# Kernel tuning notes

Hardware: AMD Instinct MI355X
Metric: run time of the kernel (lower is better)

Reference implementation:

```python
import jax, jax.numpy as jnp
import numpy as np

MAX_REL = 30
N_HEADS = 8


def conv1d(x, w, b=None, groups=1):
    # x: [B, L, Cin], w: [Cout, Cin/groups, K]  (torch Conv1d layout), 'same' padding
    pad = w.shape[-1] // 2
    y = jax.lax.conv_general_dilated(
        x, w, window_strides=(1,), padding=[(pad, pad)],
        dimension_numbers=("NLC", "OIL", "NLC"), feature_group_count=groups)
    return y if b is None else y + b


def setup_inputs() -> dict:
    key = jax.random.key(0)
    ks = jax.random.split(key, 16)
    B, L, S = 8, 1024, 512          # L = 2 * S (required by Gamma.repeat(1,2,1))
    sd, vd, dm = 512, 64, 512       # spatial_dim == d_model (residual add)
    D = 3 * vd                      # rel-pos / K,V channel dim

    def n(k, shape, s):
        return (jax.random.normal(k, shape, jnp.float32) * s).astype(jnp.float32)

    return {
        "x_spatial": jax.random.normal(ks[0], (B, L, sd), jnp.float32),
        "x_velocity": jax.random.normal(ks[1], (B, S, vd), jnp.float32),
        "w_gamma": n(ks[2], (dm, vd, 1), 0.05)[:, :, 0],      # conv_gamma 1x1, no bias -> [dm, vd]
        "w3": n(ks[3], (vd, vd, 3), 0.07), "b3": jnp.zeros((vd,), jnp.float32),
        "w5": n(ks[4], (vd, vd, 5), 0.05), "b5": jnp.zeros((vd,), jnp.float32),
        "w7": n(ks[5], (vd, vd, 7), 0.04), "b7": jnp.zeros((vd,), jnp.float32),
        "rel_table": n(ks[6], (2 * MAX_REL + 1, D), 0.05),    # embedding [61, 192]
        "dw_w": n(ks[7], (D, 1, 3), 0.3), "dw_b": jnp.zeros((D,), jnp.float32),
        "wq": n(ks[8], (dm, sd), 0.03),
        "wk": n(ks[9], (dm, D), 0.05),
        "wv": n(ks[10], (dm, D), 0.05),
        "fc_w": n(ks[11], (dm, dm), 0.03), "fc_b": jnp.zeros((dm,), jnp.float32),
        "ln_g": jnp.ones((dm,), jnp.float32), "ln_b": jnp.zeros((dm,), jnp.float32),
    }


def rel_pos_enc(ms, rel_table, dw_w, dw_b):
    # Math-equivalent reduction of the torch O(B*S^2*D) op:
    # output[b,j] = mean_i where(i==j, dwconv_row_i(fused)[j], fused[b,i,j])
    #            = ms[b,j] + mean_i rel[i,j] + (diag_conv[b,j] - fused[b,j,j]) / S
    B, S, D = ms.shape
    pos = jnp.arange(S)
    idx = jnp.clip(pos[None, :] - pos[:, None], -MAX_REL, MAX_REL) + MAX_REL  # [S,S]
    mean_rel = rel_table[idx].mean(axis=0)                                    # [S,D]
    # fused[b,i,j] = ms[b,j] + rel_table[idx[i,j]]; diagonal uses idx = MAX_REL,
    # its +/-1 neighbors along j use MAX_REL -/+ ... -> rel[i,i-1]=MAX_REL-1, rel[i,i+1]=MAX_REL+1
    center = ms + rel_table[MAX_REL]                                          # fused[b,i,i]
    left = jnp.pad(ms[:, :-1] + rel_table[MAX_REL - 1], ((0, 0), (1, 0), (0, 0)))   # conv zero-pads at i=0
    right = jnp.pad(ms[:, 1:] + rel_table[MAX_REL + 1], ((0, 0), (0, 1), (0, 0)))   # conv zero-pads at i=S-1
    diag_conv = dw_w[:, 0, 0] * left + dw_w[:, 0, 1] * center + dw_w[:, 0, 2] * right + dw_b
    return ms + mean_rel[None] + (diag_conv - center) / S


def reference(x_spatial, x_velocity, w_gamma, w3, b3, w5, b5, w7, b7,
              rel_table, dw_w, dw_b, wq, wk, wv, fc_w, fc_b, ln_g, ln_b):
    B, S, vd = x_velocity.shape
    _, L, _ = x_spatial.shape
    dm = wq.shape[0]
    dk = dm // N_HEADS

    gamma = jax.nn.sigmoid(jnp.einsum("bsc,dc->bsd", x_velocity, w_gamma))   # [B,S,dm]

    ms = jnp.concatenate([conv1d(x_velocity, w3, b3),
                          conv1d(x_velocity, w5, b5),
                          conv1d(x_velocity, w7, b7)], axis=-1)              # [B,S,3vd]
    x_pe = rel_pos_enc(ms, rel_table, dw_w, dw_b)                            # [B,S,3vd]

    q = jnp.einsum("blc,dc->bld", x_spatial, wq).reshape(B, L, N_HEADS, dk).transpose(0, 2, 1, 3)
    k = jnp.einsum("bsc,dc->bsd", x_pe, wk).reshape(B, S, N_HEADS, dk).transpose(0, 2, 1, 3)
    v = jnp.einsum("bsc,dc->bsd", x_pe, wv).reshape(B, S, N_HEADS, dk).transpose(0, 2, 1, 3)

    scores = jnp.einsum("bhld,bhsd->bhls", q, k) / jnp.sqrt(jnp.float32(dk))
    attn = jax.nn.softmax(scores, axis=-1)                                   # dropout: eval mode (identity)
    out = jnp.einsum("bhls,bhsd->bhld", attn, v)                             # [B,H,L,dk]
    out = out.transpose(0, 2, 1, 3).reshape(B, L, dm)
    out = out @ fc_w.T + fc_b

    out = jnp.tile(gamma, (1, 2, 1)) * out                                   # L == 2*S
    res = x_spatial + out
    mu = res.mean(-1, keepdims=True)
    var = res.var(-1, keepdims=True)
    return (res - mu) / jnp.sqrt(var + 1e-5) * ln_g + ln_b
```

## Files before the change

### kernel.cpp

```cpp
#include <hip/hip_runtime.h>
#include <hip/hip_bf16.h>

constexpr int B  = 8;
constexpr int L  = 1024;
constexpr int S  = 512;
constexpr int VD = 64;
constexpr int DM = 512;
constexpr int D3 = 192;
constexpr int H  = 8;
constexpr int DK = 64;

typedef __attribute__((ext_vector_type(8))) short s8v;
typedef __attribute__((ext_vector_type(4))) float f4v;

__device__ inline unsigned short f2b(float f) {
    unsigned int u = __builtin_bit_cast(unsigned int, f);
    u += 0x7fffu + ((u >> 16) & 1u);
    return (unsigned short)(u >> 16);
}
__device__ inline float b2f(unsigned int lo16) {
    return __builtin_bit_cast(float, lo16 << 16);
}

struct CastArgs {
    const float* src[7];
    unsigned short* dst[7];
    int n[7];
    float scale[7];
};

__global__ __launch_bounds__(256) void cast7_k(CastArgs a) {
    int id = blockIdx.y;
    const float* s = a.src[id];
    unsigned short* d = a.dst[id];
    int n = a.n[id];
    float sc = a.scale[id];
    for (long i = (long)(blockIdx.x * 256 + threadIdx.x) * 4; i < n;
         i += (long)gridDim.x * 1024) {
        float4 f = *(const float4*)(s + i);
        ushort4 o;
        o.x = f2b(f.x * sc); o.y = f2b(f.y * sc);
        o.z = f2b(f.z * sc); o.w = f2b(f.w * sc);
        *(ushort4*)(d + i) = o;
    }
}

__global__ __launch_bounds__(192) void wpe_build_k(
    const float* __restrict__ w3, const float* __restrict__ w5,
    const float* __restrict__ w7, const float* __restrict__ dw_w,
    unsigned short* __restrict__ WpeT)
{
    int n = blockIdx.x;
    int o = threadIdx.x;
    if (n >= 576) { WpeT[n * D3 + o] = 0; return; }
    int j = n >> 6, c = n & 63, delta = j - 4;
    const float* w; int KW, P, oo;
    if (o < 64)       { w = w3; KW = 3; P = 1; oo = o; }
    else if (o < 128) { w = w5; KW = 5; P = 2; oo = o - 64; }
    else              { w = w7; KW = 7; P = 3; oo = o - 128; }
    float inv = 1.0f / S;
    float mu[3] = { dw_w[o * 3 + 0] * inv,
                    1.f + (dw_w[o * 3 + 1] - 1.f) * inv,
                    dw_w[o * 3 + 2] * inv };
    float acc = 0.f;
#pragma unroll
    for (int ti = 0; ti < 3; ti++) {
        int k = delta - (ti - 1) + P;
        if (k >= 0 && k < KW) acc += mu[ti] * w[(oo * 64 + c) * KW + k];
    }
    WpeT[n * D3 + o] = f2b(acc);
}

__global__ __launch_bounds__(192) void cprime_k(
    const float* __restrict__ rel_table, const float* __restrict__ b3,
    const float* __restrict__ b5, const float* __restrict__ b7,
    const float* __restrict__ dw_w, const float* __restrict__ dw_b,
    unsigned short* __restrict__ Cp)
{
    int j = blockIdx.x;
    int d = threadIdx.x;
    float acc = 0.f;
#pragma unroll
    for (int r = 1; r < 60; r++) {
        int i = j - (r - 30);
        if (i >= 0 && i < S) acc += rel_table[r * D3 + d];
    }
    float c60 = (float)max(0, j - 29);
    float c0  = (float)max(0, (S - 30) - j);
    acc += c60 * rel_table[60 * D3 + d] + c0 * rel_table[0 * D3 + d];
    float inv = 1.0f / S;
    float mean_rel = acc * inv;

    float bo  = (d < 64) ? b3[d] : (d < 128) ? b5[d - 64] : b7[d - 128];
    float dw0 = dw_w[d * 3], dw1 = dw_w[d * 3 + 1], dw2 = dw_w[d * 3 + 2];
    float r29 = rel_table[29 * D3 + d], r30 = rel_table[30 * D3 + d],
          r31 = rel_table[31 * D3 + d];
    float alpha = 1.f + (dw1 - 1.f) * inv, beta = dw0 * inv, gamma = dw2 * inv;

    float cp = mean_rel + bo * alpha + (dw1 * r30 + dw_b[d] - r30) * inv;
    if (j > 0)     cp += beta * bo + dw0 * r29 * inv;
    if (j < S - 1) cp += gamma * bo + dw2 * r31 * inv;
    Cp[j * D3 + d] = f2b(cp);
}

template<bool BF16OUT>
__global__ __launch_bounds__(256) void gemm_bf16_nt(
    const unsigned short* __restrict__ A, const unsigned short* __restrict__ Bm,
    void* __restrict__ Cout, const float* __restrict__ bias,
    int M, int N, int K, int lda, int ldb, int ldc,
    long sAz, long sBz, long sCz)
{
    __shared__ __align__(16) unsigned short As[128 * 64];
    __shared__ __align__(16) unsigned short Bs[128 * 64];

    int z = blockIdx.z;
    A  += (long)z * sAz;
    Bm += (long)z * sBz;

    int t = threadIdx.x;
    int l = t & 63, w = t >> 6;
    int lx = l & 15, lh = l >> 4;
    int wr = w >> 1, wc = w & 1;
    int m0 = blockIdx.x * 128, n0 = blockIdx.y * 128;

    f4v acc[4][4] = {};

    for (int k0 = 0; k0 < K; k0 += 64) {
        __syncthreads();
#pragma unroll
        for (int p = 0; p < 4; p++) {
            int flat = p * 256 + t;
            int r = flat >> 3, c = flat & 7;
            s8v va = *(const s8v*)(A + (long)(m0 + r) * lda + k0 + c * 8);
            *(s8v*)(As + r * 64 + ((c ^ (r & 7)) * 8)) = va;
            s8v vb = *(const s8v*)(Bm + (long)(n0 + r) * ldb + k0 + c * 8);
            *(s8v*)(Bs + r * 64 + ((c ^ (r & 7)) * 8)) = vb;
        }
        __syncthreads();
#pragma unroll
        for (int ks = 0; ks < 2; ks++) {
            s8v af[4], bf[4];
#pragma unroll
            for (int i = 0; i < 4; i++) {
                int ra = wr * 64 + i * 16 + lx;
                af[i] = *(const s8v*)(As + ra * 64 + (((ks * 4 + lh) ^ (ra & 7)) * 8));
                int rb = wc * 64 + i * 16 + lx;
                bf[i] = *(const s8v*)(Bs + rb * 64 + (((ks * 4 + lh) ^ (rb & 7)) * 8));
            }
#pragma unroll
            for (int i = 0; i < 4; i++)
#pragma unroll
                for (int j = 0; j < 4; j++)
                    acc[i][j] = __builtin_amdgcn_mfma_f32_16x16x32_bf16(
                        af[i], bf[j], acc[i][j], 0, 0, 0);
        }
    }

#pragma unroll
    for (int i = 0; i < 4; i++) {
#pragma unroll
        for (int r = 0; r < 4; r++) {
            int m = m0 + wr * 64 + i * 16 + lh * 4 + r;
#pragma unroll
            for (int j = 0; j < 4; j++) {
                int n = n0 + wc * 64 + j * 16 + lx;
                float v = acc[i][j][r];
                if (bias) v += bias[n];
                if (BF16OUT)
                    ((unsigned short*)Cout + (long)z * sCz)[(long)m * ldc + n] = f2b(v);
                else
                    ((float*)Cout + (long)z * sCz)[(long)m * ldc + n] = v;
            }
        }
    }
}

__global__ __launch_bounds__(256) void convgemm_k(
    const unsigned short* __restrict__ xvb,
    const unsigned short* __restrict__ Weff0,
    const float* __restrict__ bias0,
    unsigned short* __restrict__ Cout0)
{
    __shared__ __align__(16) unsigned short As[128 * 64];
    __shared__ __align__(16) unsigned short Bs[128 * 64];

    int z = blockIdx.z;
    const unsigned short* Weff = Weff0 + (long)z * DM * 640;
    const float* bias2d = bias0 + (long)z * S * DM;
    unsigned short* Cout = Cout0 + (long)z * B * S * DM;

    int t = threadIdx.x;
    int l = t & 63, w = t >> 6;
    int lx = l & 15, lh = l >> 4;
    int wr = w >> 1, wc = w & 1;
    int m0 = blockIdx.x * 128, n0 = blockIdx.y * 128;
    int b = m0 >> 9, s0 = m0 & 511;

    f4v acc[4][4] = {};

    for (int j = 0; j < 9; j++) {
        __syncthreads();
#pragma unroll
        for (int p = 0; p < 4; p++) {
            int flat = p * 256 + t;
            int r = flat >> 3, c = flat & 7;
            int ss = s0 + r + j - 4;
            s8v va = {};
            if (ss >= 0 && ss < S)
                va = *(const s8v*)(xvb + ((long)b * S + ss) * VD + c * 8);
            *(s8v*)(As + r * 64 + ((c ^ (r & 7)) * 8)) = va;
            s8v vb = *(const s8v*)(Weff + (long)(n0 + r) * 640 + j * 64 + c * 8);
            *(s8v*)(Bs + r * 64 + ((c ^ (r & 7)) * 8)) = vb;
        }
        __syncthreads();
#pragma unroll
        for (int ks = 0; ks < 2; ks++) {
            s8v af[4], bf[4];
#pragma unroll
            for (int i = 0; i < 4; i++) {
                int ra = wr * 64 + i * 16 + lx;
                af[i] = *(const s8v*)(As + ra * 64 + (((ks * 4 + lh) ^ (ra & 7)) * 8));
                int rb = wc * 64 + i * 16 + lx;
                bf[i] = *(const s8v*)(Bs + rb * 64 + (((ks * 4 + lh) ^ (rb & 7)) * 8));
            }
#pragma unroll
            for (int i = 0; i < 4; i++)
#pragma unroll
                for (int jj = 0; jj < 4; jj++)
                    acc[i][jj] = __builtin_amdgcn_mfma_f32_16x16x32_bf16(
                        af[i], bf[jj], acc[i][jj], 0, 0, 0);
        }
    }

#pragma unroll
    for (int i = 0; i < 4; i++) {
#pragma unroll
        for (int r = 0; r < 4; r++) {
            int m = m0 + wr * 64 + i * 16 + lh * 4 + r;
            int s = m & 511;
#pragma unroll
            for (int jj = 0; jj < 4; jj++) {
                int n = n0 + wc * 64 + jj * 16 + lx;
                Cout[(long)m * DM + n] = f2b(acc[i][jj][r] + bias2d[(long)s * DM + n]);
            }
        }
    }
}

__global__ __launch_bounds__(256) void attn_mfma_k(
    const unsigned short* __restrict__ qb, const unsigned short* __restrict__ kb,
    const unsigned short* __restrict__ vb, unsigned short* __restrict__ ob)
{
    __shared__ __align__(16) unsigned short Qs[64 * 64];
    __shared__ __align__(16) unsigned short Ks[64 * 64];
    __shared__ __align__(16) unsigned short Vt[64 * 64];
    __shared__ __align__(16) unsigned short Ps[64 * 64];

    int lt = blockIdx.x, h = blockIdx.y, b = blockIdx.z;
    int t = threadIdx.x, l = t & 63, w = t >> 6, lx = l & 15, lh = l >> 4;

    const unsigned short* qg = qb + ((long)(b * L + lt * 64)) * DM + h * 64;
    const unsigned short* kg = kb + ((long)b * S) * DM + h * 64;
    const unsigned short* vg = vb + ((long)b * S) * DM + h * 64;

#pragma unroll
    for (int p = 0; p < 2; p++) {
        int flat = p * 256 + t;
        int r = flat >> 3, c = flat & 7;
        s8v v = *(const s8v*)(qg + (long)r * DM + c * 8);
        *(s8v*)(Qs + r * 64 + ((c ^ (r & 7)) * 8)) = v;
    }

    int kr0 = t >> 3, kc = t & 7;
    int vs = t & 63, vdq = t >> 6;
    s8v k0, k1, v0, v1;

    auto loadKV = [&](int st) {
        k0 = *(const s8v*)(kg + (long)(st * 64 + kr0) * DM + kc * 8);
        k1 = *(const s8v*)(kg + (long)(st * 64 + 32 + kr0) * DM + kc * 8);
        const unsigned short* vp = vg + (long)(st * 64 + vs) * DM + vdq * 16;
        v0 = *(const s8v*)(vp);
        v1 = *(const s8v*)(vp + 8);
    };
    auto writeKV = [&]() {
        *(s8v*)(Ks + kr0 * 64 + ((kc ^ (kr0 & 7)) * 8)) = k0;
        int r2 = 32 + kr0;
        *(s8v*)(Ks + r2 * 64 + ((kc ^ (r2 & 7)) * 8)) = k1;
#pragma unroll
        for (int e = 0; e < 8; e++) {
            int d1 = vdq * 16 + e;
            Vt[d1 * 64 + (((vs >> 3) ^ (d1 & 7)) * 8) + (vs & 7)] =
                (unsigned short)v0[e];
            int d2 = vdq * 16 + 8 + e;
            Vt[d2 * 64 + (((vs >> 3) ^ (d2 & 7)) * 8) + (vs & 7)] =
                (unsigned short)v1[e];
        }
    };

    loadKV(0);
    writeKV();
    __syncthreads();

    float lrow[4] = {0.f, 0.f, 0.f, 0.f};
    f4v oacc[4] = {};

    for (int st = 0; st < S / 64; st++) {
        if (st < S / 64 - 1) loadKV(st + 1);

        f4v pacc[4] = {};
        __builtin_amdgcn_s_setprio(1);
#pragma unroll
        for (int ks = 0; ks < 2; ks++) {
            int qr = w * 16 + lx;
            s8v a = *(const s8v*)(Qs + qr * 64 + (((ks * 4 + lh) ^ (qr & 7)) * 8));
#pragma unroll
            for (int jf = 0; jf < 4; jf++) {
                int kr = jf * 16 + lx;
                s8v bf = *(const s8v*)(Ks + kr * 64 + (((ks * 4 + lh) ^ (kr & 7)) * 8));
                pacc[jf] = __builtin_amdgcn_mfma_f32_16x16x32_bf16(a, bf, pacc[jf], 0, 0, 0);
            }
        }
        __builtin_amdgcn_s_setprio(0);

#pragma unroll
        for (int r = 0; r < 4; r++) {
            int prow = w * 16 + lh * 4 + r;
#pragma unroll
            for (int jf = 0; jf < 4; jf++) {
                float pe = __expf(pacc[jf][r]);
                lrow[r] += pe;
                int col = jf * 16 + lx;
                Ps[prow * 64 + (((col >> 3) ^ (prow & 7)) * 8) + (col & 7)] = f2b(pe);
            }
        }
        asm volatile("s_waitcnt lgkmcnt(0)" ::: "memory");

        __builtin_amdgcn_s_setprio(1);
#pragma unroll
        for (int ks2 = 0; ks2 < 2; ks2++) {
            int pr = w * 16 + lx;
            s8v pa = *(const s8v*)(Ps + pr * 64 + (((ks2 * 4 + lh) ^ (pr & 7)) * 8));
#pragma unroll
            for (int df = 0; df < 4; df++) {
                int vr = df * 16 + lx;
                s8v vf = *(const s8v*)(Vt + vr * 64 + (((ks2 * 4 + lh) ^ (vr & 7)) * 8));
                oacc[df] = __builtin_amdgcn_mfma_f32_16x16x32_bf16(pa, vf, oacc[df], 0, 0, 0);
            }
        }
        __builtin_amdgcn_s_setprio(0);
        __syncthreads();
        if (st < S / 64 - 1) {
            writeKV();
            __syncthreads();
        }
    }

    unsigned short* og = ob + ((long)(b * L + lt * 64 + w * 16)) * DM + h * 64;
#pragma unroll
    for (int r = 0; r < 4; r++) {
        float ls = lrow[r];
#pragma unroll
        for (int msk = 1; msk < 16; msk <<= 1) ls += __shfl_xor(ls, msk);
        float inv = 1.f / ls;
#pragma unroll
        for (int df = 0; df < 4; df++)
            og[(long)(lh * 4 + r) * DM + df * 16 + lx] = f2b(oacc[df][r] * inv);
    }
}

__global__ __launch_bounds__(256) void final_k(
    const float* __restrict__ xs, const unsigned short* __restrict__ fcb,
    const unsigned short* __restrict__ gb,
    const float* __restrict__ ln_g, const float* __restrict__ ln_b,
    float* __restrict__ out)
{
    int bl = blockIdx.x;
    int b = bl >> 10, lq = bl & 1023;
    int t = threadIdx.x;
    int d0 = t * 2;
    const unsigned short* g = gb + ((long)b * S + (lq & 511)) * DM;

    __shared__ float red[2][4];

    float2 xv = *(const float2*)(xs + (long)bl * DM + d0);
    unsigned int fp = *(const unsigned int*)(fcb + (long)bl * DM + d0);
    unsigned int gp = *(const unsigned int*)(g + d0);

    float fo0 = b2f(fp & 0xffffu), fo1 = b2f(fp >> 16);
    float ga0 = 1.f / (1.f + __expf(-b2f(gp & 0xffffu)));
    float ga1 = 1.f / (1.f + __expf(-b2f(gp >> 16)));
    float r0 = xv.x + ga0 * fo0;
    float r1 = xv.y + ga1 * fo1;

    float sum = r0 + r1, sumsq = r0 * r0 + r1 * r1;
#pragma unroll
    for (int msk = 1; msk < 64; msk <<= 1) {
        sum   += __shfl_xor(sum, msk);
        sumsq += __shfl_xor(sumsq, msk);
    }
    int wave = t >> 6;
    if ((t & 63) == 0) { red[0][wave] = sum; red[1][wave] = sumsq; }
    __syncthreads();
    float tot   = red[0][0] + red[0][1] + red[0][2] + red[0][3];
    float totsq = red[1][0] + red[1][1] + red[1][2] + red[1][3];

    float mu  = tot * (1.0f / DM);
    float var = totsq * (1.0f / DM) - mu * mu;
    float inv = rsqrtf(var + 1e-5f);

    float2 lg = *(const float2*)(ln_g + d0);
    float2 lb = *(const float2*)(ln_b + d0);
    float2 o;
    o.x = (r0 - mu) * inv * lg.x + lb.x;
    o.y = (r1 - mu) * inv * lg.y + lb.y;
    *(float2*)(out + (long)bl * DM + d0) = o;
}

extern "C" void kernel_launch(void* const* d_in, const int* in_sizes, int n_in,
                              void* d_out, int out_size, void* d_ws, size_t ws_size,
                              hipStream_t stream) {
    (void)in_sizes; (void)n_in; (void)out_size; (void)ws_size;

    const float* x_spatial  = (const float*)d_in[0];
    const float* x_velocity = (const float*)d_in[1];
    const float* w_gamma    = (const float*)d_in[2];
    const float* w3 = (const float*)d_in[3];
    const float* b3 = (const float*)d_in[4];
    const float* w5 = (const float*)d_in[5];
    const float* b5 = (const float*)d_in[6];
    const float* w7 = (const float*)d_in[7];
    const float* b7 = (const float*)d_in[8];
    const float* rel_table = (const float*)d_in[9];
    const float* dw_w = (const float*)d_in[10];
    const float* dw_b = (const float*)d_in[11];
    const float* wq   = (const float*)d_in[12];
    const float* wk   = (const float*)d_in[13];
    const float* wv   = (const float*)d_in[14];
    const float* fc_w = (const float*)d_in[15];
    const float* fc_b = (const float*)d_in[16];
    const float* ln_g = (const float*)d_in[17];
    const float* ln_b = (const float*)d_in[18];
    float* out = (float*)d_out;

    char* p = (char*)d_ws;
    auto alloc = [&](size_t bytes) {
        char* r = p;
        p += (bytes + 255) & ~(size_t)255;
        return r;
    };
    float* Ck           = (float*)alloc((size_t)S * DM * 4);
    float* Cv           = (float*)alloc((size_t)S * DM * 4);
    unsigned short* gamma_bf = (unsigned short*)alloc((size_t)B * S * DM * 2);
    unsigned short* fcb      = (unsigned short*)alloc((size_t)B * L * DM * 2);
    unsigned short* xs_bf   = (unsigned short*)alloc((size_t)B * L * DM * 2);
    unsigned short* xv_bf   = (unsigned short*)alloc((size_t)B * S * VD * 2);
    unsigned short* qbuf    = (unsigned short*)alloc((size_t)B * L * DM * 2);
    unsigned short* kbuf    = (unsigned short*)alloc((size_t)B * S * DM * 2);
    unsigned short* vbuf    = (unsigned short*)alloc((size_t)B * S * DM * 2);
    unsigned short* attn_bf = (unsigned short*)alloc((size_t)B * L * DM * 2);
    unsigned short* wq_bf   = (unsigned short*)alloc((size_t)DM * DM * 2);
    unsigned short* wk_bf   = (unsigned short*)alloc((size_t)DM * D3 * 2);
    unsigned short* wv_bf   = (unsigned short*)alloc((size_t)DM * D3 * 2);
    unsigned short* fcw_bf  = (unsigned short*)alloc((size_t)DM * DM * 2);
    unsigned short* wg_bf   = (unsigned short*)alloc((size_t)DM * VD * 2);
    unsigned short* WpeT    = (unsigned short*)alloc((size_t)640 * D3 * 2);
    unsigned short* Cp      = (unsigned short*)alloc((size_t)S * D3 * 2);
    unsigned short* WkEff   = (unsigned short*)alloc((size_t)DM * 640 * 2);
    unsigned short* WvEff   = (unsigned short*)alloc((size_t)DM * 640 * 2);

    CastArgs ca;
    ca.src[0] = x_spatial;  ca.dst[0] = xs_bf;  ca.n[0] = B * L * DM; ca.scale[0] = 1.f;
    ca.src[1] = x_velocity; ca.dst[1] = xv_bf;  ca.n[1] = B * S * VD; ca.scale[1] = 1.f;
    ca.src[2] = wq;         ca.dst[2] = wq_bf;  ca.n[2] = DM * DM;    ca.scale[2] = 0.125f;
    ca.src[3] = wk;         ca.dst[3] = wk_bf;  ca.n[3] = DM * D3;    ca.scale[3] = 1.f;
    ca.src[4] = wv;         ca.dst[4] = wv_bf;  ca.n[4] = DM * D3;    ca.scale[4] = 1.f;
    ca.src[5] = fc_w;       ca.dst[5] = fcw_bf; ca.n[5] = DM * DM;    ca.scale[5] = 1.f;
    ca.src[6] = w_gamma;    ca.dst[6] = wg_bf;  ca.n[6] = DM * VD;    ca.scale[6] = 1.f;
    cast7_k<<<dim3(4096, 7), 256, 0, stream>>>(ca);

    wpe_build_k<<<dim3(640), 192, 0, stream>>>(w3, w5, w7, dw_w, WpeT);
    cprime_k<<<dim3(S), 192, 0, stream>>>(rel_table, b3, b5, b7, dw_w, dw_b, Cp);

    gemm_bf16_nt<true><<<dim3(4, 5, 2), 256, 0, stream>>>(
        wk_bf, WpeT, WkEff, nullptr, DM, 640, D3, D3, D3, 640,
        (long)DM * D3, 0L, (long)DM * 640);

    gemm_bf16_nt<false><<<dim3(4, 4, 2), 256, 0, stream>>>(
        Cp, wk_bf, Ck, nullptr, S, DM, D3, D3, D3, DM,
        0L, (long)DM * D3, (long)S * DM);

    gemm_bf16_nt<true><<<dim3(32, 4), 256, 0, stream>>>(
        xv_bf, wg_bf, gamma_bf, nullptr, B * S, DM, VD, VD, VD, DM, 0L, 0L, 0L);

    gemm_bf16_nt<true><<<dim3(64, 4), 256, 0, stream>>>(
        xs_bf, wq_bf, qbuf, nullptr, B * L, DM, DM, DM, DM, DM, 0L, 0L, 0L);

    convgemm_k<<<dim3(32, 4, 2), 256, 0, stream>>>(xv_bf, WkEff, Ck, kbuf);

    attn_mfma_k<<<dim3(L / 64, H, B), 256, 0, stream>>>(qbuf, kbuf, vbuf, attn_bf);

    gemm_bf16_nt<true><<<dim3(64, 4), 256, 0, stream>>>(
        attn_bf, fcw_bf, fcb, fc_b, B * L, DM, DM, DM, DM, DM, 0L, 0L, 0L);

    final_k<<<dim3(B * L), 256, 0, stream>>>(
        x_spatial, fcb, gamma_bf, ln_g, ln_b, out);
}
```

Baseline: 231.3 us.

## Use direct global-to-LDS loads, fold log2e into Q, fuse effective-weight build

GEMM and conv-GEMM tile loads now use global_load_lds 16-byte transfers, applying the XOR swizzle on the global source address instead of staging through registers. Out-of-range conv rows read from a zeroed padding region. The softmax exponent switches to exp2 with log2(e) folded into the Q weight scale. The WpeT build and its small GEMM are replaced by one fp32 kernel that computes WkEff/WvEff directly, which saves a launch but runs a scalar inner loop.

New measurement: 320.2 us. +38.4%, slower.

```diff
diff --git a/kernel.cpp b/kernel.cpp
--- a/kernel.cpp
+++ b/kernel.cpp
@@ -20,6 +20,12 @@
 }
 __device__ inline float b2f(unsigned int lo16) {
     return __builtin_bit_cast(float, lo16 << 16);
+}
+
+__device__ __forceinline__ void gload16(const void* g, void* l) {
+    __builtin_amdgcn_global_load_lds(
+        (const __attribute__((address_space(1))) void*)g,
+        (__attribute__((address_space(3))) void*)l, 16, 0, 0);
 }
 
 struct CastArgs {
@@ -45,30 +51,57 @@
     }
 }
 
-__global__ __launch_bounds__(192) void wpe_build_k(
+__global__ __launch_bounds__(256) void build_eff_k(
     const float* __restrict__ w3, const float* __restrict__ w5,
     const float* __restrict__ w7, const float* __restrict__ dw_w,
-    unsigned short* __restrict__ WpeT)
+    const float* __restrict__ wk, const float* __restrict__ wv,
+    unsigned short* __restrict__ WEff)
 {
-    int n = blockIdx.x;
-    int o = threadIdx.x;
-    if (n >= 576) { WpeT[n * D3 + o] = 0; return; }
-    int j = n >> 6, c = n & 63, delta = j - 4;
-    const float* w; int KW, P, oo;
-    if (o < 64)       { w = w3; KW = 3; P = 1; oo = o; }
-    else if (o < 128) { w = w5; KW = 5; P = 2; oo = o - 64; }
-    else              { w = w7; KW = 7; P = 3; oo = o - 128; }
-    float inv = 1.0f / S;
-    float mu[3] = { dw_w[o * 3 + 0] * inv,
-                    1.f + (dw_w[o * 3 + 1] - 1.f) * inv,
-                    dw_w[o * 3 + 2] * inv };
-    float acc = 0.f;
-#pragma unroll
-    for (int ti = 0; ti < 3; ti++) {
-        int k = delta - (ti - 1) + P;
-        if (k >= 0 && k < KW) acc += mu[ti] * w[(oo * 64 + c) * KW + k];
-    }
-    WpeT[n * D3 + o] = f2b(acc);
+    int z = blockIdx.y;
+    unsigned short* out = WEff + (long)z * DM * 640;
+    int t = threadIdx.x;
+
+    if (blockIdx.x == 36) {
+        for (int idx = t; idx < DM * 64; idx += 256) {
+            int d = idx >> 6, c = idx & 63;
+            out[(long)d * 640 + 576 + c] = 0;
+        }
+        return;
+    }
+
+    int j  = blockIdx.x >> 2;
+    int dq = blockIdx.x & 3;
+    int delta = j - 4;
+
+    __shared__ float Wpe[192][64];
+    for (int e = t; e < 192 * 64; e += 256) {
+        int o = e >> 6, c = e & 63;
+        const float* w; int KW, P, oo;
+        if (o < 64)       { w = w3; KW = 3; P = 1; oo = o; }
+        else if (o < 128) { w = w5; KW = 5; P = 2; oo = o - 64; }
+        else              { w = w7; KW = 7; P = 3; oo = o - 128; }
+        float inv = 1.0f / S;
+        float mu0 = dw_w[o * 3 + 0] * inv;
+        float mu1 = 1.f + (dw_w[o * 3 + 1] - 1.f) * inv;
+        float mu2 = dw_w[o * 3 + 2] * inv;
+        float acc = 0.f;
+        int k;
+        k = delta + 1 + P; if (k >= 0 && k < KW) acc += mu0 * w[(oo * 64 + c) * KW + k];
+        k = delta + P;     if (k >= 0 && k < KW) acc += mu1 * w[(oo * 64 + c) * KW + k];
+        k = delta - 1 + P; if (k >= 0 && k < KW) acc += mu2 * w[(oo * 64 + c) * KW + k];
+        Wpe[o][c] = acc;
+    }
+    __syncthreads();
+
+    const float* wz = z ? wv : wk;
+    int c = t & 63, q = t >> 6;
+    for (int dd = 0; dd < 32; dd++) {
+        int d = dq * 128 + q * 32 + dd;
+        float acc = 0.f;
+        for (int o = 0; o < D3; o++)
+            acc += wz[(long)d * D3 + o] * Wpe[o][c];
+        out[(long)d * 640 + j * 64 + c] = f2b(acc);
+    }
 }
 
 __global__ __launch_bounds__(192) void cprime_k(
@@ -131,10 +164,9 @@
         for (int p = 0; p < 4; p++) {
             int flat = p * 256 + t;
             int r = flat >> 3, c = flat & 7;
-            s8v va = *(const s8v*)(A + (long)(m0 + r) * lda + k0 + c * 8);
-            *(s8v*)(As + r * 64 + ((c ^ (r & 7)) * 8)) = va;
-            s8v vb = *(const s8v*)(Bm + (long)(n0 + r) * ldb + k0 + c * 8);
-            *(s8v*)(Bs + r * 64 + ((c ^ (r & 7)) * 8)) = vb;
+            int csw = (c ^ (r & 7)) * 8;
+            gload16(A  + (long)(m0 + r) * lda + k0 + csw, As + flat * 8);
+            gload16(Bm + (long)(n0 + r) * ldb + k0 + csw, Bs + flat * 8);
         }
         __syncthreads();
 #pragma unroll
@@ -179,7 +211,8 @@
     const unsigned short* __restrict__ xvb,
     const unsigned short* __restrict__ Weff0,
     const float* __restrict__ bias0,
-    unsigned short* __restrict__ Cout0)
+    unsigned short* __restrict__ Cout0,
+    const unsigned short* __restrict__ zsrc)
 {
     __shared__ __align__(16) unsigned short As[128 * 64];
     __shared__ __align__(16) unsigned short Bs[128 * 64];
@@ -204,13 +237,12 @@
         for (int p = 0; p < 4; p++) {
             int flat = p * 256 + t;
             int r = flat >> 3, c = flat & 7;
+            int csw = (c ^ (r & 7)) * 8;
             int ss = s0 + r + j - 4;
-            s8v va = {};
-            if (ss >= 0 && ss < S)
-                va = *(const s8v*)(xvb + ((long)b * S + ss) * VD + c * 8);
-            *(s8v*)(As + r * 64 + ((c ^ (r & 7)) * 8)) = va;
-            s8v vb = *(const s8v*)(Weff + (long)(n0 + r) * 640 + j * 64 + c * 8);
-            *(s8v*)(Bs + r * 64 + ((c ^ (r & 7)) * 8)) = vb;
+            const unsigned short* asrc = (ss >= 0 && ss < S)
+                ? xvb + ((long)b * S + ss) * VD + csw : zsrc;
+            gload16(asrc, As + flat * 8);
+            gload16(Weff + (long)(n0 + r) * 640 + j * 64 + csw, Bs + flat * 8);
         }
         __syncthreads();
 #pragma unroll
@@ -327,7 +359,7 @@
             int prow = w * 16 + lh * 4 + r;
 #pragma unroll
             for (int jf = 0; jf < 4; jf++) {
-                float pe = __expf(pacc[jf][r]);
+                float pe = __builtin_amdgcn_exp2f(pacc[jf][r]);
                 lrow[r] += pe;
                 int col = jf * 16 + lx;
                 Ps[prow * 64 + (((col >> 3) ^ (prow & 7)) * 8) + (col & 7)] = f2b(pe);
@@ -463,7 +495,6 @@
     unsigned short* wv_bf   = (unsigned short*)alloc((size_t)DM * D3 * 2);
     unsigned short* fcw_bf  = (unsigned short*)alloc((size_t)DM * DM * 2);
     unsigned short* wg_bf   = (unsigned short*)alloc((size_t)DM * VD * 2);
-    unsigned short* WpeT    = (unsigned short*)alloc((size_t)640 * D3 * 2);
     unsigned short* Cp      = (unsigned short*)alloc((size_t)S * D3 * 2);
     unsigned short* WkEff   = (unsigned short*)alloc((size_t)DM * 640 * 2);
     unsigned short* WvEff   = (unsigned short*)alloc((size_t)DM * 640 * 2);
@@ -471,19 +502,16 @@
     CastArgs ca;
     ca.src[0] = x_spatial;  ca.dst[0] = xs_bf;  ca.n[0] = B * L * DM; ca.scale[0] = 1.f;
     ca.src[1] = x_velocity; ca.dst[1] = xv_bf;  ca.n[1] = B * S * VD; ca.scale[1] = 1.f;
-    ca.src[2] = wq;         ca.dst[2] = wq_bf;  ca.n[2] = DM * DM;    ca.scale[2] = 0.125f;
+    ca.src[2] = wq;         ca.dst[2] = wq_bf;  ca.n[2] = DM * DM;    ca.scale[2] = 0.125f * 1.44269504089f;
     ca.src[3] = wk;         ca.dst[3] = wk_bf;  ca.n[3] = DM * D3;    ca.scale[3] = 1.f;
     ca.src[4] = wv;         ca.dst[4] = wv_bf;  ca.n[4] = DM * D3;    ca.scale[4] = 1.f;
     ca.src[5] = fc_w;       ca.dst[5] = fcw_bf; ca.n[5] = DM * DM;    ca.scale[5] = 1.f;
     ca.src[6] = w_gamma;    ca.dst[6] = wg_bf;  ca.n[6] = DM * VD;    ca.scale[6] = 1.f;
     cast7_k<<<dim3(4096, 7), 256, 0, stream>>>(ca);
 
-    wpe_build_k<<<dim3(640), 192, 0, stream>>>(w3, w5, w7, dw_w, WpeT);
+    build_eff_k<<<dim3(37, 2), 256, 0, stream>>>(
+        w3, w5, w7, dw_w, wk, wv, WkEff);
     cprime_k<<<dim3(S), 192, 0, stream>>>(rel_table, b3, b5, b7, dw_w, dw_b, Cp);
-
-    gemm_bf16_nt<true><<<dim3(4, 5, 2), 256, 0, stream>>>(
-        wk_bf, WpeT, WkEff, nullptr, DM, 640, D3, D3, D3, 640,
-        (long)DM * D3, 0L, (long)DM * 640);
 
     gemm_bf16_nt<false><<<dim3(4, 4, 2), 256, 0, stream>>>(
         Cp, wk_bf, Ck, nullptr, S, DM, D3, D3, D3, DM,
@@ -495,7 +523,8 @@
     gemm_bf16_nt<true><<<dim3(64, 4), 256, 0, stream>>>(
         xs_bf, wq_bf, qbuf, nullptr, B * L, DM, DM, DM, DM, DM, 0L, 0L, 0L);
 
-    convgemm_k<<<dim3(32, 4, 2), 256, 0, stream>>>(xv_bf, WkEff, Ck, kbuf);
+    convgemm_k<<<dim3(32, 4, 2), 256, 0, stream>>>(
+        xv_bf, WkEff, Ck, kbuf, WkEff + 576 );
 
     attn_mfma_k<<<dim3(L / 64, H, B), 256, 0, stream>>>(qbuf, kbuf, vbuf, attn_bf);
 
```
